# Performance work log

Measured on AMD Instinct MI355X. Metric: run time of the kernel, lower is better.

Reference implementation:

```python
import jax, jax.numpy as jnp
import numpy as np

N, E, D_IN, D_OUT = 100000, 1250000, 64, 100


def setup_inputs() -> dict:
    key = jax.random.key(0)
    ks = jax.random.split(key, 12)
    inp = {
        "x": jax.random.normal(ks[0], (N, D_IN), dtype=jnp.float32),
        "edge_index": jax.random.randint(ks[1], (2, E), 0, N, dtype=jnp.int64),
        "edge_weight": jax.random.uniform(ks[2], (E,), dtype=jnp.float32),
        # ChebConv(64,100,K=1): one weight + bias
        "W10": jax.random.normal(ks[3], (D_IN, D_OUT), dtype=jnp.float32) * 0.1,
        "b1": jnp.zeros((D_OUT,), dtype=jnp.float32),
        # ChebConv(64,100,K=2)
        "W20": jax.random.normal(ks[4], (D_IN, D_OUT), dtype=jnp.float32) * 0.1,
        "W21": jax.random.normal(ks[5], (D_IN, D_OUT), dtype=jnp.float32) * 0.1,
        "b2": jnp.zeros((D_OUT,), dtype=jnp.float32),
        # ChebConv(64,100,K=3)
        "W30": jax.random.normal(ks[6], (D_IN, D_OUT), dtype=jnp.float32) * 0.1,
        "W31": jax.random.normal(ks[7], (D_IN, D_OUT), dtype=jnp.float32) * 0.1,
        "W32": jax.random.normal(ks[8], (D_IN, D_OUT), dtype=jnp.float32) * 0.1,
        "b3": jnp.zeros((D_OUT,), dtype=jnp.float32),
    }
    return inp


def _cheb_norm(edge_index, edge_weight, n):
    # PyG ChebConv.__norm__ with normalization='sym', lambda_max=2.0:
    # L_hat = (2/lambda_max) * (I - D^-1/2 A D^-1/2) - I = -D^-1/2 A D^-1/2
    # (the +1 diagonal of L and the -1 self-loop cancel), diag entries are 0.
    row, col = edge_index[0], edge_index[1]
    deg = jax.ops.segment_sum(edge_weight, row, num_segments=n)
    dis = jnp.where(deg > 0, jax.lax.rsqrt(jnp.where(deg > 0, deg, 1.0)), 0.0)
    return -dis[row] * edge_weight * dis[col]


def _cheb_conv(x, edge_index, w_hat, weights, bias):
    # out = sum_k T_k(L_hat) x @ W_k + b, with T0=x, T1=Lx, T_k=2L T_{k-1}-T_{k-2}
    n = x.shape[0]
    row, col = edge_index[0], edge_index[1]

    def prop(t):  # L_hat @ t via edge gather/scatter
        return jax.ops.segment_sum(t[row] * w_hat[:, None], col, num_segments=n)

    tx0 = x
    out = tx0 @ weights[0]
    if len(weights) > 1:
        tx1 = prop(tx0)
        out = out + tx1 @ weights[1]
        for k in range(2, len(weights)):
            tx2 = 2.0 * prop(tx1) - tx0
            out = out + tx2 @ weights[k]
            tx0, tx1 = tx1, tx2
    return out + bias


def reference(x, edge_index, edge_weight, W10, b1, W20, W21, b2, W30, W31, W32, b3):
    w_hat = _cheb_norm(edge_index, edge_weight, x.shape[0])
    s1 = _cheb_conv(x, edge_index, w_hat, [W10], b1)
    s2 = _cheb_conv(x, edge_index, w_hat, [W20, W21], b2)
    s3 = _cheb_conv(x, edge_index, w_hat, [W30, W31, W32], b3)
    return jnp.concatenate([s1, s2, s3], axis=1)  # [N, 300]
```

## Files before the change

### kernel.cpp

```cpp
#include <hip/hip_runtime.h>


typedef __attribute__((ext_vector_type(8))) short short8;
typedef __attribute__((ext_vector_type(8))) unsigned short ushort8;
typedef __attribute__((ext_vector_type(4))) float f32x4;

#define CAP 48

__device__ inline float bf2f(unsigned short u) {
    return __uint_as_float(((unsigned int)u) << 16);
}
__device__ inline unsigned short f2bf(float f) {
    unsigned int u = __float_as_uint(f);
    u = (u + 0x7FFF + ((u >> 16) & 1)) >> 16;
    return (unsigned short)u;
}

__global__ void scatter_bucket_kernel(const int* __restrict__ row, const int* __restrict__ col,
                                      const float* __restrict__ ew, float* __restrict__ deg,
                                      int* __restrict__ cursor, uint2* __restrict__ erec, int E) {
    int e = blockIdx.x * 256 + threadIdx.x;
    if (e < E) {
        int r = row[e], c = col[e];
        float w = ew[e];
        atomicAdd(&deg[r], w);
        int p = atomicAdd(&cursor[c], 1);
        if (p < CAP) erec[(size_t)c * CAP + p] = make_uint2((unsigned)r, __float_as_uint(w));
    }
}

__global__ void deg_count_kernel(const int* __restrict__ row, const int* __restrict__ col,
                                 const float* __restrict__ ew,
                                 float* __restrict__ deg, int* __restrict__ cnt, int E) {
    int e = blockIdx.x * 256 + threadIdx.x;
    if (e < E) {
        atomicAdd(&deg[row[e]], ew[e]);
        atomicAdd(&cnt[col[e]], 1);
    }
}

__global__ void scan1_kernel(const int* __restrict__ cnt, int* __restrict__ pre,
                             int* __restrict__ bsum, int N) {
    __shared__ int s[256];
    int t = threadIdx.x;
    int i = blockIdx.x * 256 + t;
    int v = (i < N) ? cnt[i] : 0;
    s[t] = v;
    __syncthreads();
    for (int o = 1; o < 256; o <<= 1) {
        int u = (t >= o) ? s[t - o] : 0;
        __syncthreads();
        s[t] += u;
        __syncthreads();
    }
    if (i < N) pre[i] = s[t] - v;
    if (t == 255) bsum[blockIdx.x] = s[255];
}

__global__ void scan2_kernel(const int* __restrict__ bsum, int* __restrict__ bpre, int nb) {
    __shared__ int s[512];
    int t = threadIdx.x;
    int v = (t < nb) ? bsum[t] : 0;
    s[t] = v;
    __syncthreads();
    for (int o = 1; o < 512; o <<= 1) {
        int u = (t >= o) ? s[t - o] : 0;
        __syncthreads();
        s[t] += u;
        __syncthreads();
    }
    if (t < nb) bpre[t] = s[t] - v;
}

__global__ void scan3_kernel(int* __restrict__ rowptr, int* __restrict__ cursor,
                             const int* __restrict__ bpre, int N, int E) {
    int i = blockIdx.x * 256 + threadIdx.x;
    if (i < N) {
        int v = rowptr[i] + bpre[i >> 8];
        rowptr[i] = v;
        cursor[i] = v;
    }
    if (i == 0) rowptr[N] = E;
}

__global__ void scatter_compact_kernel(const int* __restrict__ row, const int* __restrict__ col,
                                       const float* __restrict__ ew, int* __restrict__ cursor,
                                       uint2* __restrict__ erec, int E) {
    int e = blockIdx.x * 256 + threadIdx.x;
    if (e < E) {
        int p = atomicAdd(&cursor[col[e]], 1);
        erec[p] = make_uint2((unsigned)row[e], __float_as_uint(ew[e]));
    }
}

__global__ void cvt_dis_kernel(const float* __restrict__ x, unsigned short* __restrict__ xb,
                               float* __restrict__ deg_dis, int N, int total4) {
    int i = blockIdx.x * 256 + threadIdx.x;
    if (i < total4) {
        float4 v = reinterpret_cast<const float4*>(x)[i];
        ushort4 o;
        o.x = f2bf(v.x); o.y = f2bf(v.y); o.z = f2bf(v.z); o.w = f2bf(v.w);
        reinterpret_cast<ushort4*>(xb)[i] = o;
    }
    if (i < N) {
        float d = deg_dis[i];
        deg_dis[i] = (d > 0.f) ? rsqrtf(d) : 0.f;
    }
}

__global__ void gather_kernel(const int* __restrict__ ptr, const int* __restrict__ cnt,
                              const uint2* __restrict__ erec, const float* __restrict__ dis,
                              const unsigned short* __restrict__ src,
                              unsigned short* __restrict__ dst, int N, int cap) {
    int node = blockIdx.x * 4 + (threadIdx.x >> 6);
    int lane = threadIdx.x & 63;
    if (node >= N) return;
    int s, d;
    if (cap > 0) {
        s = node * cap;
        d = min(cnt[node], cap);
    } else {
        s = ptr[node];
        d = ptr[node + 1] - s;
    }
    float acc = 0.f;
    for (int base = 0; base < d; base += 64) {
        int n = min(64, d - base);
        uint2 e = make_uint2(0u, 0u);
        float w = 0.f;
        if (lane < n) {
            e = erec[s + base + lane];
            w = __uint_as_float(e.y) * dis[e.x];
        }
        int n4 = (n + 3) & ~3;
        for (int j = 0; j < n4; j += 4) {
            int r0 = __shfl((int)e.x, j + 0, 64);
            int r1 = __shfl((int)e.x, j + 1, 64);
            int r2 = __shfl((int)e.x, j + 2, 64);
            int r3 = __shfl((int)e.x, j + 3, 64);
            float w0 = __shfl(w, j + 0, 64);
            float w1 = __shfl(w, j + 1, 64);
            float w2 = __shfl(w, j + 2, 64);
            float w3 = __shfl(w, j + 3, 64);
            float v0 = bf2f(src[(size_t)r0 * 64 + lane]);
            float v1 = bf2f(src[(size_t)r1 * 64 + lane]);
            float v2 = bf2f(src[(size_t)r2 * 64 + lane]);
            float v3 = bf2f(src[(size_t)r3 * 64 + lane]);
            acc = fmaf(w0, v0, acc);
            acc = fmaf(w1, v1, acc);
            acc = fmaf(w2, v2, acc);
            acc = fmaf(w3, v3, acc);
        }
    }
    dst[(size_t)node * 64 + lane] = f2bf(-dis[node] * acc);
}

__global__ void prep_w_kernel(const float* __restrict__ W10, const float* __restrict__ W20,
                              const float* __restrict__ W21, const float* __restrict__ W30,
                              const float* __restrict__ W31, const float* __restrict__ W32,
                              unsigned short* __restrict__ imgW) {
    int i = blockIdx.x * 256 + threadIdx.x;
    if (i >= 6 * 7168) return;
    int img = i / 7168;
    int rem = i - img * 7168;
    int colc = rem >> 6;
    int k = rem & 63;
    const float* W;
    switch (img) {
        case 0: W = W10; break;
        case 1: W = W20; break;
        case 2: W = W21; break;
        case 3: W = W30; break;
        case 4: W = W31; break;
        default: W = W32; break;
    }
    float v = (colc < 100) ? W[k * 100 + colc] : 0.f;
    int g = k >> 3, j = k & 7;
    imgW[img * 7168 + colc * 64 + ((g ^ (colc & 7)) << 3) + j] = f2bf(v);
}

__global__ __launch_bounds__(256) void gemm_mfma_kernel(
        const unsigned short* __restrict__ xb, const unsigned short* __restrict__ tx1b,
        const unsigned short* __restrict__ p2b, const unsigned short* __restrict__ imgW,
        const float* __restrict__ b1, const float* __restrict__ b2,
        const float* __restrict__ b3, float* __restrict__ out, int N) {
    __shared__ unsigned short Ft[64 * 64];
    __shared__ unsigned short Ws[112 * 64];
    const int bid = blockIdx.x;
    const int seg = bid % 3;
    const int tile = bid / 3;
    const int row0 = tile * 64;
    const int tid = threadIdx.x;
    const int wv = tid >> 6;
    const int l = tid & 63;
    const int m = l & 15;
    const int q = l >> 4;

    f32x4 acc[7];
#pragma unroll
    for (int t = 0; t < 7; ++t) acc[t] = (f32x4){0.f, 0.f, 0.f, 0.f};

    const int imgBase = (seg * (seg + 1) / 2) * 7168;

    for (int c = 0; c <= seg; ++c) {
        const unsigned short* __restrict__ src = (c == 0) ? xb : (c == 1) ? tx1b : p2b;
#pragma unroll
        for (int it = 0; it < 2; ++it) {
            int i = tid + it * 256;
            int r = i >> 3, g = i & 7;
            int grow = row0 + r;
            ushort8 v = {0, 0, 0, 0, 0, 0, 0, 0};
            if (grow < N) {
                v = *reinterpret_cast<const ushort8*>(src + (size_t)grow * 64 + g * 8);
                if (c == 2) {
                    ushort8 xv = *reinterpret_cast<const ushort8*>(xb + (size_t)grow * 64 + g * 8);
#pragma unroll
                    for (int jj = 0; jj < 8; ++jj)
                        v[jj] = f2bf(2.f * bf2f(v[jj]) - bf2f(xv[jj]));
                }
            }
            *reinterpret_cast<ushort8*>(&Ft[r * 64 + ((g ^ (r & 7)) << 3)]) = v;
        }
        const uint4* wsrc = reinterpret_cast<const uint4*>(imgW + imgBase + c * 7168);
        uint4* wdst = reinterpret_cast<uint4*>(Ws);
#pragma unroll
        for (int it = 0; it < 4; ++it) {
            int i = tid + it * 256;
            if (i < 896) wdst[i] = wsrc[i];
        }
        __syncthreads();

        const int arow = wv * 16 + m;
#pragma unroll
        for (int ks = 0; ks < 2; ++ks) {
            short8 a = *reinterpret_cast<const short8*>(
                &Ft[arow * 64 + (((ks * 4 + q) ^ (arow & 7)) << 3)]);
#pragma unroll
            for (int t = 0; t < 7; ++t) {
                int n = t * 16 + m;
                short8 b = *reinterpret_cast<const short8*>(
                    &Ws[n * 64 + (((ks * 4 + q) ^ (n & 7)) << 3)]);
                acc[t] = __builtin_amdgcn_mfma_f32_16x16x32_bf16(a, b, acc[t], 0, 0, 0);
            }
        }
        __syncthreads();
    }

    const float* bsel = (seg == 0) ? b1 : (seg == 1) ? b2 : b3;
#pragma unroll
    for (int t = 0; t < 7; ++t) {
        int colseg = t * 16 + m;
        if (colseg >= 100) continue;
        float bv = bsel[colseg];
#pragma unroll
        for (int i = 0; i < 4; ++i) {
            int grow = row0 + wv * 16 + q * 4 + i;
            if (grow < N) out[(size_t)grow * 300 + seg * 100 + colseg] = acc[t][i] + bv;
        }
    }
}

extern "C" void kernel_launch(void* const* d_in, const int* in_sizes, int n_in,
                              void* d_out, int out_size, void* d_ws, size_t ws_size,
                              hipStream_t stream) {
    const float* x   = (const float*)d_in[0];
    const int*   ei  = (const int*)d_in[1];
    const float* ew  = (const float*)d_in[2];
    const float* W10 = (const float*)d_in[3];
    const float* b1  = (const float*)d_in[4];
    const float* W20 = (const float*)d_in[5];
    const float* W21 = (const float*)d_in[6];
    const float* b2  = (const float*)d_in[7];
    const float* W30 = (const float*)d_in[8];
    const float* W31 = (const float*)d_in[9];
    const float* W32 = (const float*)d_in[10];
    const float* b3  = (const float*)d_in[11];
    float* out = (float*)d_out;

    const int N = in_sizes[0] / 64;
    const int E = in_sizes[2];
    const int* row = ei;
    const int* col = ei + E;
    const int nb = (N + 255) / 256;
    const int eb = (E + 255) / 256;

    char* base = (char*)d_ws;
    size_t off = 0;
    auto alloc = [&](size_t bytes) { size_t o = off; off = (off + bytes + 15) & ~(size_t)15; return o; };

    float* deg           = (float*)(base + alloc((size_t)4 * N));
    int*   cursor        = (int*)(base + alloc((size_t)4 * N));
    unsigned short* xb   = (unsigned short*)(base + alloc((size_t)128 * N));
    unsigned short* tx1b = (unsigned short*)(base + alloc((size_t)128 * N));
    unsigned short* p2b  = (unsigned short*)(base + alloc((size_t)128 * N));
    unsigned short* imgW = (unsigned short*)(base + alloc((size_t)2 * 6 * 7168));
    size_t common = off;

    size_t need_bucket = common + (size_t)8 * N * CAP + 64;
    int total4 = N * 16;
    int pg = (N + 3) / 4;
    int ntile = (N + 63) / 64;

    if (need_bucket <= ws_size) {
        uint2* erec = (uint2*)(base + alloc((size_t)8 * N * CAP));

        hipMemsetAsync(deg, 0, (size_t)8 * N, stream);
        scatter_bucket_kernel<<<eb, 256, 0, stream>>>(row, col, ew, deg, cursor, erec, E);
        cvt_dis_kernel<<<(total4 + 255) / 256, 256, 0, stream>>>(x, xb, deg, N, total4);
        prep_w_kernel<<<(6 * 7168 + 255) / 256, 256, 0, stream>>>(W10, W20, W21, W30, W31, W32, imgW);

        gather_kernel<<<pg, 256, 0, stream>>>(nullptr, cursor, erec, deg, xb, tx1b, N, CAP);
        gather_kernel<<<pg, 256, 0, stream>>>(nullptr, cursor, erec, deg, tx1b, p2b, N, CAP);
        gemm_mfma_kernel<<<ntile * 3, 256, 0, stream>>>(xb, tx1b, p2b, imgW, b1, b2, b3, out, N);
    } else {
        int*   rowptr = (int*)(base + alloc((size_t)4 * (N + 1)));
        int*   bsum   = (int*)(base + alloc((size_t)4 * nb));
        int*   bpre   = (int*)(base + alloc((size_t)4 * nb));
        uint2* erec   = (uint2*)(base + alloc((size_t)8 * E));

        hipMemsetAsync(deg, 0, (size_t)8 * N, stream);
        deg_count_kernel<<<eb, 256, 0, stream>>>(row, col, ew, deg, cursor, E);
        scan1_kernel<<<nb, 256, 0, stream>>>(cursor, rowptr, bsum, N);
        scan2_kernel<<<1, 512, 0, stream>>>(bsum, bpre, nb);
        scan3_kernel<<<nb, 256, 0, stream>>>(rowptr, cursor, bpre, N, E);
        scatter_compact_kernel<<<eb, 256, 0, stream>>>(row, col, ew, cursor, erec, E);
        cvt_dis_kernel<<<(total4 + 255) / 256, 256, 0, stream>>>(x, xb, deg, N, total4);
        prep_w_kernel<<<(6 * 7168 + 255) / 256, 256, 0, stream>>>(W10, W20, W21, W30, W31, W32, imgW);

        gather_kernel<<<pg, 256, 0, stream>>>(rowptr, nullptr, erec, deg, xb, tx1b, N, 0);
        gather_kernel<<<pg, 256, 0, stream>>>(rowptr, nullptr, erec, deg, tx1b, p2b, N, 0);
        gemm_mfma_kernel<<<ntile * 3, 256, 0, stream>>>(xb, tx1b, p2b, imgW, b1, b2, b3, out, N);
    }
}
```

Before: 442.8 us.

## Privatize degree and bucket atomics per XCD to avoid cross-die atomic traffic

The scatter stage now keeps separate degree sums, counters and edge buckets for each XCD, chosen by reading the hardware XCC_ID register. It uses workgroup-scope relaxed atomics so updates can stay in the local L2 instead of going through device-wide coherent atomics, and it vectorizes the edge reads four at a time. The gather kernel merges the eight sub-buckets through a prefix of their counts, and the dis computation sums the eight partial degrees. In exchange, the counter and degree arrays grow eightfold, the gather needs extra index arithmetic, and correctness depends on every workgroup on one XCD sharing an L2, since workgroup-scope atomics are not formally coherent across workgroups.

```diff
diff --git a/kernel.cpp b/kernel.cpp
--- a/kernel.cpp
+++ b/kernel.cpp
@@ -4,8 +4,6 @@
 typedef __attribute__((ext_vector_type(8))) short short8;
 typedef __attribute__((ext_vector_type(8))) unsigned short ushort8;
 typedef __attribute__((ext_vector_type(4))) float f32x4;
-
-#define CAP 48
 
 __device__ inline float bf2f(unsigned short u) {
     return __uint_as_float(((unsigned int)u) << 16);
@@ -16,16 +14,64 @@
     return (unsigned short)u;
 }
 
-__global__ void scatter_bucket_kernel(const int* __restrict__ row, const int* __restrict__ col,
-                                      const float* __restrict__ ew, float* __restrict__ deg,
-                                      int* __restrict__ cursor, uint2* __restrict__ erec, int E) {
+__device__ inline unsigned xcc_id() {
+    unsigned x;
+    asm("s_getreg_b32 %0, hwreg(HW_REG_XCC_ID)" : "=s"(x));
+    return x & 7u;
+}
+
+__device__ inline float atomAddL(float* p, float v) {
+    return __hip_atomic_fetch_add(p, v, __ATOMIC_RELAXED, __HIP_MEMORY_SCOPE_WORKGROUP);
+}
+__device__ inline int atomAddL(int* p, int v) {
+    return __hip_atomic_fetch_add(p, v, __ATOMIC_RELAXED, __HIP_MEMORY_SCOPE_WORKGROUP);
+}
+
+__global__ void scatter_xcd4_kernel(const int* __restrict__ row, const int* __restrict__ col,
+                                    const float* __restrict__ ew, float* __restrict__ deg8,
+                                    int* __restrict__ cnt8, uint2* __restrict__ erec,
+                                    int E, int capx) {
+    const unsigned xcd = xcc_id();
+    int e0 = (blockIdx.x * 256 + threadIdx.x) * 4;
+    if (e0 + 3 < E) {
+        int4 r = *reinterpret_cast<const int4*>(row + e0);
+        int4 c = *reinterpret_cast<const int4*>(col + e0);
+        float4 w = *reinterpret_cast<const float4*>(ew + e0);
+        atomAddL(&deg8[(size_t)r.x * 8 + xcd], w.x);
+        atomAddL(&deg8[(size_t)r.y * 8 + xcd], w.y);
+        atomAddL(&deg8[(size_t)r.z * 8 + xcd], w.z);
+        atomAddL(&deg8[(size_t)r.w * 8 + xcd], w.w);
+        int p0 = atomAddL(&cnt8[(size_t)c.x * 8 + xcd], 1);
+        int p1 = atomAddL(&cnt8[(size_t)c.y * 8 + xcd], 1);
+        int p2 = atomAddL(&cnt8[(size_t)c.z * 8 + xcd], 1);
+        int p3 = atomAddL(&cnt8[(size_t)c.w * 8 + xcd], 1);
+        if (p0 < capx) erec[((size_t)c.x * 8 + xcd) * capx + p0] = make_uint2((unsigned)r.x, __float_as_uint(w.x));
+        if (p1 < capx) erec[((size_t)c.y * 8 + xcd) * capx + p1] = make_uint2((unsigned)r.y, __float_as_uint(w.y));
+        if (p2 < capx) erec[((size_t)c.z * 8 + xcd) * capx + p2] = make_uint2((unsigned)r.z, __float_as_uint(w.z));
+        if (p3 < capx) erec[((size_t)c.w * 8 + xcd) * capx + p3] = make_uint2((unsigned)r.w, __float_as_uint(w.w));
+    } else if (e0 < E) {
+        for (int e = e0; e < E; ++e) {
+            int r = row[e], c = col[e];
+            float w = ew[e];
+            atomAddL(&deg8[(size_t)r * 8 + xcd], w);
+            int p = atomAddL(&cnt8[(size_t)c * 8 + xcd], 1);
+            if (p < capx) erec[((size_t)c * 8 + xcd) * capx + p] = make_uint2((unsigned)r, __float_as_uint(w));
+        }
+    }
+}
+
+__global__ void scatter_xcd1_kernel(const int* __restrict__ row, const int* __restrict__ col,
+                                    const float* __restrict__ ew, float* __restrict__ deg8,
+                                    int* __restrict__ cnt8, uint2* __restrict__ erec,
+                                    int E, int capx) {
+    const unsigned xcd = xcc_id();
     int e = blockIdx.x * 256 + threadIdx.x;
     if (e < E) {
         int r = row[e], c = col[e];
         float w = ew[e];
-        atomicAdd(&deg[r], w);
-        int p = atomicAdd(&cursor[c], 1);
-        if (p < CAP) erec[(size_t)c * CAP + p] = make_uint2((unsigned)r, __float_as_uint(w));
+        atomAddL(&deg8[(size_t)r * 8 + xcd], w);
+        int p = atomAddL(&cnt8[(size_t)c * 8 + xcd], 1);
+        if (p < capx) erec[((size_t)c * 8 + xcd) * capx + p] = make_uint2((unsigned)r, __float_as_uint(w));
     }
 }
 
@@ -94,7 +140,8 @@
 }
 
 __global__ void cvt_dis_kernel(const float* __restrict__ x, unsigned short* __restrict__ xb,
-                               float* __restrict__ deg_dis, int N, int total4) {
+                               const float* __restrict__ deg, float* __restrict__ dis,
+                               int N, int total4, int dstride) {
     int i = blockIdx.x * 256 + threadIdx.x;
     if (i < total4) {
         float4 v = reinterpret_cast<const float4*>(x)[i];
@@ -103,53 +150,94 @@
         reinterpret_cast<ushort4*>(xb)[i] = o;
     }
     if (i < N) {
-        float d = deg_dis[i];
-        deg_dis[i] = (d > 0.f) ? rsqrtf(d) : 0.f;
-    }
-}
-
-__global__ void gather_kernel(const int* __restrict__ ptr, const int* __restrict__ cnt,
+        float d;
+        if (dstride == 8) {
+            float4 a = reinterpret_cast<const float4*>(deg)[i * 2];
+            float4 b = reinterpret_cast<const float4*>(deg)[i * 2 + 1];
+            d = ((a.x + a.y) + (a.z + a.w)) + ((b.x + b.y) + (b.z + b.w));
+        } else {
+            d = deg[i];
+        }
+        dis[i] = (d > 0.f) ? rsqrtf(d) : 0.f;
+    }
+}
+
+__device__ inline void chunk_fma(int ex, float w, int n, int lane,
+                                 const unsigned short* __restrict__ src, float& acc) {
+    int n4 = (n + 3) & ~3;
+    for (int j = 0; j < n4; j += 4) {
+        int r0 = __shfl(ex, j + 0, 64);
+        int r1 = __shfl(ex, j + 1, 64);
+        int r2 = __shfl(ex, j + 2, 64);
+        int r3 = __shfl(ex, j + 3, 64);
+        float w0 = __shfl(w, j + 0, 64);
+        float w1 = __shfl(w, j + 1, 64);
+        float w2 = __shfl(w, j + 2, 64);
+        float w3 = __shfl(w, j + 3, 64);
+        float v0 = bf2f(src[(size_t)r0 * 64 + lane]);
+        float v1 = bf2f(src[(size_t)r1 * 64 + lane]);
+        float v2 = bf2f(src[(size_t)r2 * 64 + lane]);
+        float v3 = bf2f(src[(size_t)r3 * 64 + lane]);
+        acc = fmaf(w0, v0, acc);
+        acc = fmaf(w1, v1, acc);
+        acc = fmaf(w2, v2, acc);
+        acc = fmaf(w3, v3, acc);
+    }
+}
+
+__global__ void gather_kernel(const int* __restrict__ ptr, const int* __restrict__ cnt8,
                               const uint2* __restrict__ erec, const float* __restrict__ dis,
                               const unsigned short* __restrict__ src,
-                              unsigned short* __restrict__ dst, int N, int cap) {
+                              unsigned short* __restrict__ dst, int N, int xcdmode, int capx) {
     int node = blockIdx.x * 4 + (threadIdx.x >> 6);
     int lane = threadIdx.x & 63;
     if (node >= N) return;
-    int s, d;
-    if (cap > 0) {
-        s = node * cap;
-        d = min(cnt[node], cap);
+    float acc = 0.f;
+    if (xcdmode) {
+        int4 ca = *reinterpret_cast<const int4*>(cnt8 + (size_t)node * 8);
+        int4 cb = *reinterpret_cast<const int4*>(cnt8 + (size_t)node * 8 + 4);
+        int p1 = min(ca.x, capx);
+        int p2 = p1 + min(ca.y, capx);
+        int p3 = p2 + min(ca.z, capx);
+        int p4 = p3 + min(ca.w, capx);
+        int p5 = p4 + min(cb.x, capx);
+        int p6 = p5 + min(cb.y, capx);
+        int p7 = p6 + min(cb.z, capx);
+        int d  = p7 + min(cb.w, capx);
+        const uint2* eb = erec + (size_t)node * 8 * capx;
+        for (int base = 0; base < d; base += 64) {
+            int n = min(64, d - base);
+            int ex = 0;
+            float w = 0.f;
+            int flat = base + lane;
+            if (flat < d) {
+                int k = 0, pk = 0;
+                if (flat >= p1) { k = 1; pk = p1; }
+                if (flat >= p2) { k = 2; pk = p2; }
+                if (flat >= p3) { k = 3; pk = p3; }
+                if (flat >= p4) { k = 4; pk = p4; }
+                if (flat >= p5) { k = 5; pk = p5; }
+                if (flat >= p6) { k = 6; pk = p6; }
+                if (flat >= p7) { k = 7; pk = p7; }
+                uint2 e = eb[k * capx + (flat - pk)];
+                ex = (int)e.x;
+                w = __uint_as_float(e.y) * dis[ex];
+            }
+            chunk_fma(ex, w, n, lane, src, acc);
+        }
     } else {
-        s = ptr[node];
-        d = ptr[node + 1] - s;
-    }
-    float acc = 0.f;
-    for (int base = 0; base < d; base += 64) {
-        int n = min(64, d - base);
-        uint2 e = make_uint2(0u, 0u);
-        float w = 0.f;
-        if (lane < n) {
-            e = erec[s + base + lane];
-            w = __uint_as_float(e.y) * dis[e.x];
-        }
-        int n4 = (n + 3) & ~3;
-        for (int j = 0; j < n4; j += 4) {
-            int r0 = __shfl((int)e.x, j + 0, 64);
-            int r1 = __shfl((int)e.x, j + 1, 64);
-            int r2 = __shfl((int)e.x, j + 2, 64);
-            int r3 = __shfl((int)e.x, j + 3, 64);
-            float w0 = __shfl(w, j + 0, 64);
-            float w1 = __shfl(w, j + 1, 64);
-            float w2 = __shfl(w, j + 2, 64);
-            float w3 = __shfl(w, j + 3, 64);
-            float v0 = bf2f(src[(size_t)r0 * 64 + lane]);
-            float v1 = bf2f(src[(size_t)r1 * 64 + lane]);
-            float v2 = bf2f(src[(size_t)r2 * 64 + lane]);
-            float v3 = bf2f(src[(size_t)r3 * 64 + lane]);
-            acc = fmaf(w0, v0, acc);
-            acc = fmaf(w1, v1, acc);
-            acc = fmaf(w2, v2, acc);
-            acc = fmaf(w3, v3, acc);
+        int s = ptr[node];
+        int d = ptr[node + 1] - s;
+        for (int base = 0; base < d; base += 64) {
+            int n = min(64, d - base);
+            int ex = 0;
+            float w = 0.f;
+            if (lane < n) {
+                uint2 e = erec[s + base + lane];
+                ex = (int)e.x;
+                w = __uint_as_float(e.y) * dis[ex];
+            }
+            chunk_fma(ex, w, n, lane, src, acc);
         }
     }
     dst[(size_t)node * 64 + lane] = f2bf(-dis[node] * acc);
@@ -288,47 +376,59 @@
     size_t off = 0;
     auto alloc = [&](size_t bytes) { size_t o = off; off = (off + bytes + 15) & ~(size_t)15; return o; };
 
-    float* deg           = (float*)(base + alloc((size_t)4 * N));
-    int*   cursor        = (int*)(base + alloc((size_t)4 * N));
+    float* dis           = (float*)(base + alloc((size_t)4 * N));
+    float* deg8          = (float*)(base + alloc((size_t)32 * N));
+    int*   cnt8          = (int*)(base + alloc((size_t)32 * N));
     unsigned short* xb   = (unsigned short*)(base + alloc((size_t)128 * N));
     unsigned short* tx1b = (unsigned short*)(base + alloc((size_t)128 * N));
     unsigned short* p2b  = (unsigned short*)(base + alloc((size_t)128 * N));
     unsigned short* imgW = (unsigned short*)(base + alloc((size_t)2 * 6 * 7168));
     size_t common = off;
 
-    size_t need_bucket = common + (size_t)8 * N * CAP + 64;
     int total4 = N * 16;
     int pg = (N + 3) / 4;
     int ntile = (N + 63) / 64;
 
-    if (need_bucket <= ws_size) {
-        uint2* erec = (uint2*)(base + alloc((size_t)8 * N * CAP));
-
-        hipMemsetAsync(deg, 0, (size_t)8 * N, stream);
-        scatter_bucket_kernel<<<eb, 256, 0, stream>>>(row, col, ew, deg, cursor, erec, E);
-        cvt_dis_kernel<<<(total4 + 255) / 256, 256, 0, stream>>>(x, xb, deg, N, total4);
+    int capx = 0;
+    if (common + (size_t)8 * N * 8 * 16 + 64 <= ws_size) capx = 16;
+    else if (common + (size_t)8 * N * 8 * 12 + 64 <= ws_size) capx = 12;
+
+    if (capx > 0) {
+        uint2* erec = (uint2*)(base + alloc((size_t)8 * N * 8 * capx));
+
+        hipMemsetAsync(deg8, 0, (size_t)64 * N, stream);
+        if ((E & 3) == 0) {
+            int ebv = (E / 4 + 255) / 256;
+            scatter_xcd4_kernel<<<ebv, 256, 0, stream>>>(row, col, ew, deg8, cnt8, erec, E, capx);
+        } else {
+            scatter_xcd1_kernel<<<eb, 256, 0, stream>>>(row, col, ew, deg8, cnt8, erec, E, capx);
+        }
+        cvt_dis_kernel<<<(total4 + 255) / 256, 256, 0, stream>>>(x, xb, deg8, dis, N, total4, 8);
         prep_w_kernel<<<(6 * 7168 + 255) / 256, 256, 0, stream>>>(W10, W20, W21, W30, W31, W32, imgW);
 
-        gather_kernel<<<pg, 256, 0, stream>>>(nullptr, cursor, erec, deg, xb, tx1b, N, CAP);
-        gather_kernel<<<pg, 256, 0, stream>>>(nullptr, cursor, erec, deg, tx1b, p2b, N, CAP);
+        gather_kernel<<<pg, 256, 0, stream>>>(nullptr, cnt8, erec, dis, xb, tx1b, N, 1, capx);
+        gather_kernel<<<pg, 256, 0, stream>>>(nullptr, cnt8, erec, dis, tx1b, p2b, N, 1, capx);
         gemm_mfma_kernel<<<ntile * 3, 256, 0, stream>>>(xb, tx1b, p2b, imgW, b1, b2, b3, out, N);
     } else {
+        float* deg    = deg8;
+        int*   cursor = cnt8;
         int*   rowptr = (int*)(base + alloc((size_t)4 * (N + 1)));
         int*   bsum   = (int*)(base + alloc((size_t)4 * nb));
         int*   bpre   = (int*)(base + alloc((size_t)4 * nb));
         uint2* erec   = (uint2*)(base + alloc((size_t)8 * E));
 
-        hipMemsetAsync(deg, 0, (size_t)8 * N, stream);
+        hipMemsetAsync(deg, 0, (size_t)4 * N, stream);
+        hipMemsetAsync(cursor, 0, (size_t)4 * N, stream);
         deg_count_kernel<<<eb, 256, 0, stream>>>(row, col, ew, deg, cursor, E);
         scan1_kernel<<<nb, 256, 0, stream>>>(cursor, rowptr, bsum, N);
         scan2_kernel<<<1, 512, 0, stream>>>(bsum, bpre, nb);
         scan3_kernel<<<nb, 256, 0, stream>>>(rowptr, cursor, bpre, N, E);
         scatter_compact_kernel<<<eb, 256, 0, stream>>>(row, col, ew, cursor, erec, E);
-        cvt_dis_kernel<<<(total4 + 255) / 256, 256, 0, stream>>>(x, xb, deg, N, total4);
+        cvt_dis_kernel<<<(total4 + 255) / 256, 256, 0, stream>>>(x, xb, deg, dis, N, total4, 1);
         prep_w_kernel<<<(6 * 7168 + 255) / 256, 256, 0, stream>>>(W10, W20, W21, W30, W31, W32, imgW);
 
-        gather_kernel<<<pg, 256, 0, stream>>>(rowptr, nullptr, erec, deg, xb, tx1b, N, 0);
-        gather_kernel<<<pg, 256, 0, stream>>>(rowptr, nullptr, erec, deg, tx1b, p2b, N, 0);
+        gather_kernel<<<pg, 256, 0, stream>>>(rowptr, nullptr, erec, dis, xb, tx1b, N, 0, 0);
+        gather_kernel<<<pg, 256, 0, stream>>>(rowptr, nullptr, erec, dis, tx1b, p2b, N, 0, 0);
         gemm_mfma_kernel<<<ntile * 3, 256, 0, stream>>>(xb, tx1b, p2b, imgW, b1, b2, b3, out, N);
     }
 }
```

Result: slower. 475.8 us (+7.4%).

## Replace per-node atomic bucketing with two-level LDS-histogram partition into CSR

Applied to the files above, without the earlier changes.

Graph preprocessing now partitions edges into coarse 256-node buckets, using per-block LDS histograms to reserve global space. Per-bucket kernels then compute degrees and the rsqrt normalization in shared memory and build a compact CSR sorted by column, with the source-node normalization folded into the edge weights. This replaces the per-node global atomics and padded 48-slot buckets, which cost heavy atomic contention and wasted bandwidth, and lets the gathers skip the dis[] lookup. It adds several launches and an intermediate partition buffer, and edges beyond CAPB per bucket would be silently dropped.

```diff
diff --git a/kernel.cpp b/kernel.cpp
--- a/kernel.cpp
+++ b/kernel.cpp
@@ -5,7 +5,8 @@
 typedef __attribute__((ext_vector_type(8))) unsigned short ushort8;
 typedef __attribute__((ext_vector_type(4))) float f32x4;
 
-#define CAP 48
+#define CAPB 8192
+#define MAXBUCK 512
 
 __device__ inline float bf2f(unsigned short u) {
     return __uint_as_float(((unsigned int)u) << 16);
@@ -16,16 +17,120 @@
     return (unsigned short)u;
 }
 
-__global__ void scatter_bucket_kernel(const int* __restrict__ row, const int* __restrict__ col,
-                                      const float* __restrict__ ew, float* __restrict__ deg,
-                                      int* __restrict__ cursor, uint2* __restrict__ erec, int E) {
-    int e = blockIdx.x * 256 + threadIdx.x;
-    if (e < E) {
-        int r = row[e], c = col[e];
-        float w = ew[e];
-        atomicAdd(&deg[r], w);
-        int p = atomicAdd(&cursor[c], 1);
-        if (p < CAP) erec[(size_t)c * CAP + p] = make_uint2((unsigned)r, __float_as_uint(w));
+__global__ __launch_bounds__(256) void part_kernel(
+        const int* __restrict__ row, const int* __restrict__ col,
+        const float* __restrict__ ew, int* __restrict__ colcur,
+        int* __restrict__ rowcur, uint2* __restrict__ colpart,
+        uint2* __restrict__ rowpart, int E, int nbuck, int chunk) {
+    __shared__ int hc[MAXBUCK];
+    __shared__ int hr[MAXBUCK];
+    const int t = threadIdx.x;
+    const int s = blockIdx.x * chunk;
+    const int e = min(E, s + chunk);
+    if (s >= E) return;
+    for (int i = t; i < nbuck; i += 256) { hc[i] = 0; hr[i] = 0; }
+    __syncthreads();
+    for (int i = s + t; i < e; i += 256) {
+        atomicAdd(&hc[col[i] >> 8], 1);
+        atomicAdd(&hr[row[i] >> 8], 1);
+    }
+    __syncthreads();
+    for (int i = t; i < nbuck; i += 256) {
+        int n = hc[i];
+        hc[i] = n ? atomicAdd(&colcur[i], n) : 0;
+        n = hr[i];
+        hr[i] = n ? atomicAdd(&rowcur[i], n) : 0;
+    }
+    __syncthreads();
+    for (int i = s + t; i < e; i += 256) {
+        int r = row[i], c = col[i];
+        float w = ew[i];
+        int cb = c >> 8, rb = r >> 8;
+        int pc = atomicAdd(&hc[cb], 1);
+        if (pc < CAPB)
+            colpart[(size_t)cb * CAPB + pc] =
+                make_uint2(((unsigned)(c & 255) << 24) | (unsigned)r, __float_as_uint(w));
+        int pr = atomicAdd(&hr[rb], 1);
+        if (pr < CAPB)
+            rowpart[(size_t)rb * CAPB + pr] = make_uint2((unsigned)r, __float_as_uint(w));
+    }
+}
+
+__global__ __launch_bounds__(256) void fine_row_kernel(
+        const int* __restrict__ rowcur, const uint2* __restrict__ rowpart,
+        float* __restrict__ dis, int N) {
+    __shared__ float s[256];
+    const int b = blockIdx.x, t = threadIdx.x;
+    const int sz = min(rowcur[b], CAPB);
+    const uint2* part = rowpart + (size_t)b * CAPB;
+    s[t] = 0.f;
+    __syncthreads();
+    for (int i = t; i < sz; i += 256) {
+        uint2 rec = part[i];
+        atomicAdd(&s[rec.x & 255u], __uint_as_float(rec.y));
+    }
+    __syncthreads();
+    int r = (b << 8) + t;
+    if (r < N) {
+        float d = s[t];
+        dis[r] = (d > 0.f) ? rsqrtf(d) : 0.f;
+    }
+}
+
+__global__ void colbase_scan_kernel(const int* __restrict__ colcur,
+                                    int* __restrict__ colbase,
+                                    int* __restrict__ rowptr, int N, int nbuck) {
+    __shared__ int s[MAXBUCK];
+    int t = threadIdx.x;
+    int v = (t < nbuck) ? min(colcur[t], CAPB) : 0;
+    s[t] = v;
+    __syncthreads();
+    for (int o = 1; o < MAXBUCK; o <<= 1) {
+        int u = (t >= o) ? s[t - o] : 0;
+        __syncthreads();
+        s[t] += u;
+        __syncthreads();
+    }
+    if (t < nbuck) colbase[t] = s[t] - v;
+    if (t == MAXBUCK - 1) rowptr[N] = s[MAXBUCK - 1];
+}
+
+__global__ __launch_bounds__(256) void fine_col_kernel(
+        const int* __restrict__ colcur, const int* __restrict__ colbase,
+        const uint2* __restrict__ colpart, const float* __restrict__ dis,
+        uint2* __restrict__ erec, int* __restrict__ rowptr, int N) {
+    __shared__ int h[256];
+    __shared__ int sc[256];
+    __shared__ int cur[256];
+    const int b = blockIdx.x, t = threadIdx.x;
+    const int sz = min(colcur[b], CAPB);
+    const uint2* part = colpart + (size_t)b * CAPB;
+    h[t] = 0;
+    __syncthreads();
+    for (int i = t; i < sz; i += 256) atomicAdd(&h[part[i].x >> 24], 1);
+    __syncthreads();
+    int v = h[t];
+    sc[t] = v;
+    __syncthreads();
+    for (int o = 1; o < 256; o <<= 1) {
+        int u = (t >= o) ? sc[t - o] : 0;
+        __syncthreads();
+        sc[t] += u;
+        __syncthreads();
+    }
+    int excl = sc[t] - v;
+    const int base = colbase[b];
+    int c = (b << 8) + t;
+    if (c < N) rowptr[c] = base + excl;
+    cur[t] = excl;
+    __syncthreads();
+    for (int i = t; i < sz; i += 256) {
+        uint2 rec = part[i];
+        int coff = rec.x >> 24;
+        int r = rec.x & 0xFFFFFFu;
+        int pos = atomicAdd(&cur[coff], 1);
+        float wd = __uint_as_float(rec.y) * dis[r];
+        erec[(size_t)base + pos] = make_uint2((unsigned)r, __float_as_uint(wd));
     }
 }
 
@@ -94,7 +199,8 @@
 }
 
 __global__ void cvt_dis_kernel(const float* __restrict__ x, unsigned short* __restrict__ xb,
-                               float* __restrict__ deg_dis, int N, int total4) {
+                               const float* __restrict__ deg, float* __restrict__ dis,
+                               int N, int total4, int dodis) {
     int i = blockIdx.x * 256 + threadIdx.x;
     if (i < total4) {
         float4 v = reinterpret_cast<const float4*>(x)[i];
@@ -102,42 +208,38 @@
         o.x = f2bf(v.x); o.y = f2bf(v.y); o.z = f2bf(v.z); o.w = f2bf(v.w);
         reinterpret_cast<ushort4*>(xb)[i] = o;
     }
-    if (i < N) {
-        float d = deg_dis[i];
-        deg_dis[i] = (d > 0.f) ? rsqrtf(d) : 0.f;
-    }
-}
-
-__global__ void gather_kernel(const int* __restrict__ ptr, const int* __restrict__ cnt,
-                              const uint2* __restrict__ erec, const float* __restrict__ dis,
+    if (dodis && i < N) {
+        float d = deg[i];
+        dis[i] = (d > 0.f) ? rsqrtf(d) : 0.f;
+    }
+}
+
+__global__ void gather_kernel(const int* __restrict__ ptr, const uint2* __restrict__ erec,
+                              const float* __restrict__ dis,
                               const unsigned short* __restrict__ src,
-                              unsigned short* __restrict__ dst, int N, int cap) {
+                              unsigned short* __restrict__ dst, int N, int premul) {
     int node = blockIdx.x * 4 + (threadIdx.x >> 6);
     int lane = threadIdx.x & 63;
     if (node >= N) return;
-    int s, d;
-    if (cap > 0) {
-        s = node * cap;
-        d = min(cnt[node], cap);
-    } else {
-        s = ptr[node];
-        d = ptr[node + 1] - s;
-    }
+    int s = ptr[node];
+    int d = ptr[node + 1] - s;
     float acc = 0.f;
     for (int base = 0; base < d; base += 64) {
         int n = min(64, d - base);
-        uint2 e = make_uint2(0u, 0u);
+        int ex = 0;
         float w = 0.f;
         if (lane < n) {
-            e = erec[s + base + lane];
-            w = __uint_as_float(e.y) * dis[e.x];
+            uint2 e = erec[s + base + lane];
+            ex = (int)e.x;
+            w = __uint_as_float(e.y);
+            if (!premul) w *= dis[ex];
         }
         int n4 = (n + 3) & ~3;
         for (int j = 0; j < n4; j += 4) {
-            int r0 = __shfl((int)e.x, j + 0, 64);
-            int r1 = __shfl((int)e.x, j + 1, 64);
-            int r2 = __shfl((int)e.x, j + 2, 64);
-            int r3 = __shfl((int)e.x, j + 3, 64);
+            int r0 = __shfl(ex, j + 0, 64);
+            int r1 = __shfl(ex, j + 1, 64);
+            int r2 = __shfl(ex, j + 2, 64);
+            int r3 = __shfl(ex, j + 3, 64);
             float w0 = __shfl(w, j + 0, 64);
             float w1 = __shfl(w, j + 1, 64);
             float w2 = __shfl(w, j + 2, 64);
@@ -283,52 +385,70 @@
     const int* col = ei + E;
     const int nb = (N + 255) / 256;
     const int eb = (E + 255) / 256;
+    const int nbuck = (N + 255) >> 8;
+
+    int total4 = N * 16;
+    int pg = (N + 3) / 4;
+    int ntile = (N + 63) / 64;
 
     char* base = (char*)d_ws;
     size_t off = 0;
     auto alloc = [&](size_t bytes) { size_t o = off; off = (off + bytes + 15) & ~(size_t)15; return o; };
 
-    float* deg           = (float*)(base + alloc((size_t)4 * N));
-    int*   cursor        = (int*)(base + alloc((size_t)4 * N));
+    float* dis           = (float*)(base + alloc((size_t)4 * N));
+    int*   rowptr        = (int*)(base + alloc((size_t)4 * (N + 1)));
+    int*   colcur        = (int*)(base + alloc((size_t)4 * MAXBUCK * 2));
+    int*   rowcur        = colcur + MAXBUCK;
+    int*   colbase       = (int*)(base + alloc((size_t)4 * MAXBUCK));
     unsigned short* xb   = (unsigned short*)(base + alloc((size_t)128 * N));
     unsigned short* tx1b = (unsigned short*)(base + alloc((size_t)128 * N));
     unsigned short* p2b  = (unsigned short*)(base + alloc((size_t)128 * N));
     unsigned short* imgW = (unsigned short*)(base + alloc((size_t)2 * 6 * 7168));
-    size_t common = off;
-
-    size_t need_bucket = common + (size_t)8 * N * CAP + 64;
-    int total4 = N * 16;
-    int pg = (N + 3) / 4;
-    int ntile = (N + 63) / 64;
-
-    if (need_bucket <= ws_size) {
-        uint2* erec = (uint2*)(base + alloc((size_t)8 * N * CAP));
-
-        hipMemsetAsync(deg, 0, (size_t)8 * N, stream);
-        scatter_bucket_kernel<<<eb, 256, 0, stream>>>(row, col, ew, deg, cursor, erec, E);
-        cvt_dis_kernel<<<(total4 + 255) / 256, 256, 0, stream>>>(x, xb, deg, N, total4);
+    uint2* erec          = (uint2*)(base + alloc((size_t)8 * E));
+    size_t mainfix = off;
+    uint2* colpart       = (uint2*)(base + alloc((size_t)8 * nbuck * CAPB));
+    uint2* rowpart       = (uint2*)(base + alloc((size_t)8 * nbuck * CAPB));
+    size_t mainneed = off;
+
+    bool mainok = (N < (1 << 24)) && (nbuck <= MAXBUCK) && (mainneed <= ws_size);
+
+    if (mainok) {
+        const int PBLK = 512;
+        int chunk = (E + PBLK - 1) / PBLK;
+
+        hipMemsetAsync(colcur, 0, (size_t)4 * MAXBUCK * 2, stream);
+        part_kernel<<<PBLK, 256, 0, stream>>>(row, col, ew, colcur, rowcur,
+                                              colpart, rowpart, E, nbuck, chunk);
+        fine_row_kernel<<<nbuck, 256, 0, stream>>>(rowcur, rowpart, dis, N);
+        colbase_scan_kernel<<<1, MAXBUCK, 0, stream>>>(colcur, colbase, rowptr, N, nbuck);
+        fine_col_kernel<<<nbuck, 256, 0, stream>>>(colcur, colbase, colpart, dis,
+                                                   erec, rowptr, N);
+        cvt_dis_kernel<<<(total4 + 255) / 256, 256, 0, stream>>>(x, xb, nullptr, nullptr,
+                                                                 N, total4, 0);
         prep_w_kernel<<<(6 * 7168 + 255) / 256, 256, 0, stream>>>(W10, W20, W21, W30, W31, W32, imgW);
 
-        gather_kernel<<<pg, 256, 0, stream>>>(nullptr, cursor, erec, deg, xb, tx1b, N, CAP);
-        gather_kernel<<<pg, 256, 0, stream>>>(nullptr, cursor, erec, deg, tx1b, p2b, N, CAP);
+        gather_kernel<<<pg, 256, 0, stream>>>(rowptr, erec, dis, xb, tx1b, N, 1);
+        gather_kernel<<<pg, 256, 0, stream>>>(rowptr, erec, dis, tx1b, p2b, N, 1);
         gemm_mfma_kernel<<<ntile * 3, 256, 0, stream>>>(xb, tx1b, p2b, imgW, b1, b2, b3, out, N);
     } else {
-        int*   rowptr = (int*)(base + alloc((size_t)4 * (N + 1)));
+        off = mainfix;
+        float* deg    = (float*)(base + alloc((size_t)4 * N));
+        int*   cursor = (int*)(base + alloc((size_t)4 * N));
         int*   bsum   = (int*)(base + alloc((size_t)4 * nb));
         int*   bpre   = (int*)(base + alloc((size_t)4 * nb));
-        uint2* erec   = (uint2*)(base + alloc((size_t)8 * E));
-
-        hipMemsetAsync(deg, 0, (size_t)8 * N, stream);
+
+        hipMemsetAsync(deg, 0, (size_t)4 * N, stream);
+        hipMemsetAsync(cursor, 0, (size_t)4 * N, stream);
         deg_count_kernel<<<eb, 256, 0, stream>>>(row, col, ew, deg, cursor, E);
         scan1_kernel<<<nb, 256, 0, stream>>>(cursor, rowptr, bsum, N);
         scan2_kernel<<<1, 512, 0, stream>>>(bsum, bpre, nb);
         scan3_kernel<<<nb, 256, 0, stream>>>(rowptr, cursor, bpre, N, E);
         scatter_compact_kernel<<<eb, 256, 0, stream>>>(row, col, ew, cursor, erec, E);
-        cvt_dis_kernel<<<(total4 + 255) / 256, 256, 0, stream>>>(x, xb, deg, N, total4);
+        cvt_dis_kernel<<<(total4 + 255) / 256, 256, 0, stream>>>(x, xb, deg, dis, N, total4, 1);
         prep_w_kernel<<<(6 * 7168 + 255) / 256, 256, 0, stream>>>(W10, W20, W21, W30, W31, W32, imgW);
 
-        gather_kernel<<<pg, 256, 0, stream>>>(rowptr, nullptr, erec, deg, xb, tx1b, N, 0);
-        gather_kernel<<<pg, 256, 0, stream>>>(rowptr, nullptr, erec, deg, tx1b, p2b, N, 0);
+        gather_kernel<<<pg, 256, 0, stream>>>(rowptr, erec, dis, xb, tx1b, N, 0);
+        gather_kernel<<<pg, 256, 0, stream>>>(rowptr, erec, dis, tx1b, p2b, N, 0);
         gemm_mfma_kernel<<<ntile * 3, 256, 0, stream>>>(xb, tx1b, p2b, imgW, b1, b2, b3, out, N);
     }
 }
```

Measured after the change: 414.1 us. -6.5%, faster.
